# Optimization experiments

Measured on AMD Instinct MI355X. Metric: run time of the kernel, lower is better.

Reference implementation:

```python
import jax, jax.numpy as jnp
import numpy as np

B, S, D, H = 4, 2048, 1024, 16
DH = D // H


def setup_inputs() -> dict:
    key = jax.random.key(0)
    ks = jax.random.split(key, 10)
    init = lambda k, shape: jax.random.normal(k, shape, dtype=jnp.float32) * 0.02
    return {
        "x": jax.random.normal(ks[0], (B, S, D), dtype=jnp.float32),
        "attention_mask": jnp.ones((B, S), dtype=bool),
        "use_causal_mask": 1,
        "Wq": init(ks[1], (D, D)), "bq": jnp.zeros((D,), jnp.float32),
        "Wk": init(ks[2], (D, D)), "bk": jnp.zeros((D,), jnp.float32),
        "Wv": init(ks[3], (D, D)), "bv": jnp.zeros((D,), jnp.float32),
        "Wo": init(ks[4], (D, D)), "bo": jnp.zeros((D,), jnp.float32),
    }


def _split_heads(t):
    # (B, S, D) -> (B, H, S, DH)
    b, s, d = t.shape
    return t.reshape(b, s, H, DH).transpose(0, 2, 1, 3)


def reference(x, attention_mask, use_causal_mask, Wq, bq, Wk, bk, Wv, bv, Wo, bo):
    q = _split_heads(x @ Wq + bq)  # (B, H, S, DH)
    k = _split_heads(x @ Wk + bk)
    v = _split_heads(x @ Wv + bv)

    scale = 1.0 / jnp.sqrt(jnp.asarray(DH, dtype=x.dtype))
    scores = jnp.einsum("bhqd,bhkd->bhqk", q, k) * scale  # (B, H, S, S)

    blocked = jnp.finfo(scores.dtype).min
    if use_causal_mask:
        causal = jnp.tril(jnp.ones((S, S), dtype=bool))[None, None]
        scores = jnp.where(causal, scores, blocked)
    # attention_mask: (B, S) over keys
    scores = jnp.where(attention_mask[:, None, None, :], scores, blocked)

    weights = jax.nn.softmax(scores, axis=-1)
    attn = jnp.einsum("bhqk,bhkd->bhqd", weights, v)  # (B, H, S, DH)
    attn = attn.transpose(0, 2, 1, 3).reshape(B, S, D)  # combine heads
    return attn @ Wo + bo
```

## Files before the change

kernel.cpp:

```cpp
#include <hip/hip_runtime.h>
#include <hip/hip_bf16.h>
#include <cstdint>
#include <cstddef>


#define BB 4
#define SS 2048
#define DD 1024
#define HH 16
#define DHH 64

typedef float f32x4 __attribute__((ext_vector_type(4)));
typedef __bf16 bf16x8 __attribute__((ext_vector_type(8)));

#define QSCALE 0.1803368801111204f

__device__ __forceinline__ unsigned short f2bf(float f) {
  union { __hip_bfloat16 h; unsigned short u; } cv;
  cv.h = __float2bfloat16(f);
  return cv.u;
}

__device__ __forceinline__ float fexp2(float x) { return __builtin_amdgcn_exp2f(x); }

__device__ __forceinline__ void gload_lds16(const void* g, void* l) {
  __builtin_amdgcn_global_load_lds((const __attribute__((address_space(1))) void*)g,
                                   (__attribute__((address_space(3))) void*)l,
                                   16, 0, 0);
}

__global__ void k_f32_to_bf16(const float* __restrict__ in,
                              unsigned short* __restrict__ out, int n8) {
  int i = blockIdx.x * blockDim.x + threadIdx.x;
  if (i >= n8) return;
  const float4* p = (const float4*)in + (size_t)i * 2;
  float4 a = p[0], b = p[1];
  union { unsigned short u[8]; uint4 v; } r;
  r.u[0] = f2bf(a.x); r.u[1] = f2bf(a.y); r.u[2] = f2bf(a.z); r.u[3] = f2bf(a.w);
  r.u[4] = f2bf(b.x); r.u[5] = f2bf(b.y); r.u[6] = f2bf(b.z); r.u[7] = f2bf(b.w);
  ((uint4*)out)[i] = r.v;
}

__global__ void k_transpose_w4(const float* __restrict__ Wq, const float* __restrict__ Wk,
                               const float* __restrict__ Wv, const float* __restrict__ Wo,
                               unsigned short* __restrict__ Wqkvt,
                               unsigned short* __restrict__ Wot) {
  __shared__ float t[64][65];
  const int z = blockIdx.z;
  const float* W = (z == 0) ? Wq : (z == 1) ? Wk : (z == 2) ? Wv : Wo;
  unsigned short* dst = (z < 3) ? (Wqkvt + (size_t)z * DD * DD) : Wot;
  int bx = blockIdx.x * 64;
  int by = blockIdx.y * 64;
  int c  = threadIdx.x & 63;
  int r0 = threadIdx.x >> 6;
#pragma unroll
  for (int r = r0; r < 64; r += 4)
    t[r][c] = W[(size_t)(by + r) * DD + bx + c];
  __syncthreads();
#pragma unroll
  for (int r = r0; r < 64; r += 4)
    dst[(size_t)(bx + r) * DD + by + c] = f2bf(t[c][r]);
}

template <int MODE, int GN>
__global__ __launch_bounds__(256) void k_gemm(const unsigned short* __restrict__ A,
                                              const unsigned short* __restrict__ Bt,
                                              const float* __restrict__ b0,
                                              const float* __restrict__ b1,
                                              const float* __restrict__ b2,
                                              void* __restrict__ out0,
                                              void* __restrict__ out1,
                                              void* __restrict__ out2) {
  constexpr int Kd = 1024;
  __shared__ unsigned short As[128 * 64];
  __shared__ unsigned short Bs[128 * 64];
  const int tid = threadIdx.x;
  const int wave = tid >> 6, lane = tid & 63;
  const int hw = blockIdx.x;
  const int xcd = hw & 7;
  const int j = hw >> 3;
  const int super = j >> 6;
  const int rem = j & 63;
  const int bm = (xcd * 8 + (rem >> 3)) * 128;
  const int bn = (super * 8 + (rem & 7)) * 128;
  const int wm = (wave >> 1) * 64, wn = (wave & 1) * 64;

  f32x4 acc[4][4] = {};

  const int srow = wave * 8 + (lane >> 3);
  const int csw = lane & 7;

  for (int k0 = 0; k0 < Kd; k0 += 64) {
#pragma unroll
    for (int q = 0; q < 4; q++) {
      int r = q * 32 + srow;
      int clog = csw ^ (r & 7);
      gload_lds16(A + (size_t)(bm + r) * Kd + k0 + clog * 8, &As[q * 2048 + wave * 512]);
      gload_lds16(Bt + (size_t)(bn + r) * Kd + k0 + clog * 8, &Bs[q * 2048 + wave * 512]);
    }
    __syncthreads();
#pragma unroll
    for (int kk = 0; kk < 2; kk++) {
      bf16x8 af[4], bfr[4];
      int ch = (kk << 2) | (lane >> 4);
#pragma unroll
      for (int i = 0; i < 4; i++) {
        int row = wm + i * 16 + (lane & 15);
        af[i] = *(const bf16x8*)&As[row * 64 + ((ch ^ (row & 7)) << 3)];
      }
#pragma unroll
      for (int j2 = 0; j2 < 4; j2++) {
        int col = wn + j2 * 16 + (lane & 15);
        bfr[j2] = *(const bf16x8*)&Bs[col * 64 + ((ch ^ (col & 7)) << 3)];
      }
#pragma unroll
      for (int i = 0; i < 4; i++)
#pragma unroll
        for (int j2 = 0; j2 < 4; j2++)
          acc[i][j2] = __builtin_amdgcn_mfma_f32_16x16x32_bf16(af[i], bfr[j2], acc[i][j2], 0, 0, 0);
    }
    __syncthreads();
  }

  const int mat = bn >> 10;
  const float* bias = (MODE == 2) ? b0 : (mat == 0 ? b0 : (mat == 1 ? b1 : b2));
  const float scale = (MODE == 0 && mat == 0) ? QSCALE : 1.0f;
#pragma unroll
  for (int i = 0; i < 4; i++) {
#pragma unroll
    for (int j2 = 0; j2 < 4; j2++) {
      int col = bn + wn + j2 * 16 + (lane & 15);
      int c2 = col & 1023;
      float bv = bias[MODE == 2 ? col : c2];
      int row0 = bm + wm + i * 16 + ((lane >> 4) << 2);
      if (MODE == 0 && mat == 2) {
        int b = row0 >> 11, s0 = row0 & 2047, h = c2 >> 6, dh = c2 & 63;
        ushort4 pk;
        pk.x = f2bf(acc[i][j2][0] + bv);
        pk.y = f2bf(acc[i][j2][1] + bv);
        pk.z = f2bf(acc[i][j2][2] + bv);
        pk.w = f2bf(acc[i][j2][3] + bv);
        *(ushort4*)((unsigned short*)out2 + (((size_t)(b * HH + h) * DHH + dh) << 11) + s0) = pk;
      } else {
#pragma unroll
        for (int reg = 0; reg < 4; reg++) {
          int row = row0 + reg;
          float v = (acc[i][j2][reg] + bv) * scale;
          if (MODE == 0) {
            int b = row >> 11, s = row & 2047, h = c2 >> 6, dh = c2 & 63;
            unsigned short* dst = (unsigned short*)(mat == 0 ? out0 : out1);
            dst[(((size_t)(b * HH + h) * SS + s) << 6) + dh] = f2bf(v);
          } else {
            ((float*)out0)[(size_t)row * DD + col] = v;
          }
        }
      }
    }
  }
}

__global__ __launch_bounds__(256) void k_attn(const unsigned short* __restrict__ Q,
                                              const unsigned short* __restrict__ Kb,
                                              const unsigned short* __restrict__ Vt,
                                              unsigned short* __restrict__ O,
                                              const int* __restrict__ use_causal) {
  __shared__ unsigned short Ks[64 * 64];
  __shared__ unsigned short Vs[64 * 64];
  __shared__ unsigned short Ps[4 * 16 * 64];
  const int hw = blockIdx.x;
  const int bh = (hw & 7) | ((hw >> 7) << 3);
  const int pr = (hw >> 3) & 15;
  const int b = bh >> 4, h = bh & 15;
  const int tid = threadIdx.x, wave = tid >> 6, lane = tid & 63;
  const int lanelo = lane & 15, lanehi = lane >> 4;
  const bool causal = (use_causal[0] != 0);

  const unsigned short* Kg = Kb + (size_t)bh * SS * DHH;
  const unsigned short* Vg = Vt + (size_t)bh * DHH * SS;
  const int srow = wave * 8 + (lane >> 3);
  const int csw = lane & 7;
  const int qlocal = wave * 16 + lanelo;

  for (int pass = 0; pass < 2; pass++) {
    const int qt = pass ? (SS / 64 - 1 - pr) : pr;
    const unsigned short* Qg = Q + ((size_t)bh * SS + qt * 64) * DHH;

    bf16x8 qf0, qf1;
    {
      const unsigned short* qrow = Qg + (wave * 16 + lanelo) * DHH + (lanehi << 3);
      qf0 = *(const bf16x8*)qrow;
      qf1 = *(const bf16x8*)(qrow + 32);
    }

    float m = -1e30f, ls = 0.f;
    f32x4 o[4] = {};
    const int ntile = causal ? (qt + 1) : (SS / 64);

    for (int kt = 0; kt < ntile; kt++) {
#pragma unroll
      for (int q = 0; q < 2; q++) {
        int r = q * 32 + srow;
        int clog = csw ^ (r & 7);
        gload_lds16(Kg + (size_t)(kt * 64 + r) * DHH + clog * 8, &Ks[q * 2048 + wave * 512]);
        gload_lds16(Vg + (size_t)r * SS + kt * 64 + clog * 8, &Vs[q * 2048 + wave * 512]);
      }
      __syncthreads();

      f32x4 scT[4];
#pragma unroll
      for (int kb = 0; kb < 4; kb++) {
        int key = kb * 16 + lanelo;
        bf16x8 a0 = *(const bf16x8*)&Ks[key * 64 + ((lanehi ^ (key & 7)) << 3)];
        bf16x8 a1 = *(const bf16x8*)&Ks[key * 64 + (((lanehi + 4) ^ (key & 7)) << 3)];
        f32x4 t = {};
        t = __builtin_amdgcn_mfma_f32_16x16x32_bf16(a0, qf0, t, 0, 0, 0);
        t = __builtin_amdgcn_mfma_f32_16x16x32_bf16(a1, qf1, t, 0, 0, 0);
        scT[kb] = t;
      }

      const bool needmask = causal && (kt == qt);
      float mx = -3.0e38f;
#pragma unroll
      for (int kb = 0; kb < 4; kb++)
#pragma unroll
        for (int reg = 0; reg < 4; reg++) {
          float v = scT[kb][reg];
          if (needmask && (kb * 16 + 4 * lanehi + reg) > qlocal) v = -3.0e38f;
          scT[kb][reg] = v;
          mx = fmaxf(mx, v);
        }

      if (__any((int)(mx > m + 8.0f))) {
        float rmx = fmaxf(mx, __shfl_xor(mx, 16, 64));
        rmx = fmaxf(rmx, __shfl_xor(rmx, 32, 64));
        float mnew = fmaxf(m, rmx);
        float al = fexp2(m - mnew);
        m = mnew;
        ls *= al;
        float alr[4];
#pragma unroll
        for (int reg = 0; reg < 4; reg++)
          alr[reg] = __shfl(al, (lanehi << 2) + reg, 64);
#pragma unroll
        for (int dhb = 0; dhb < 4; dhb++) {
          f32x4 t = o[dhb];
          t[0] *= alr[0]; t[1] *= alr[1]; t[2] *= alr[2]; t[3] *= alr[3];
          o[dhb] = t;
        }
      }

      unsigned short* Pw = &Ps[wave * 1024];
#pragma unroll
      for (int kb = 0; kb < 4; kb++) {
        ushort4 pk;
        float p0 = fexp2(scT[kb][0] - m);
        float p1 = fexp2(scT[kb][1] - m);
        float p2 = fexp2(scT[kb][2] - m);
        float p3 = fexp2(scT[kb][3] - m);
        ls += (p0 + p1) + (p2 + p3);
        pk.x = f2bf(p0); pk.y = f2bf(p1); pk.z = f2bf(p2); pk.w = f2bf(p3);
        int chunk = (kb * 2 + (lanehi >> 1)) ^ (lanelo & 7);
        *(ushort4*)&Pw[lanelo * 64 + (chunk << 3) + ((lanehi & 1) << 2)] = pk;
      }

      int ar = lanelo;
      bf16x8 pa0 = *(const bf16x8*)&Pw[ar * 64 + ((lanehi ^ (ar & 7)) << 3)];
      bf16x8 pa1 = *(const bf16x8*)&Pw[ar * 64 + (((lanehi + 4) ^ (ar & 7)) << 3)];
#pragma unroll
      for (int dhb = 0; dhb < 4; dhb++) {
        int dh = dhb * 16 + lanelo;
        bf16x8 v0 = *(const bf16x8*)&Vs[dh * 64 + ((lanehi ^ (dh & 7)) << 3)];
        bf16x8 v1 = *(const bf16x8*)&Vs[dh * 64 + (((lanehi + 4) ^ (dh & 7)) << 3)];
        o[dhb] = __builtin_amdgcn_mfma_f32_16x16x32_bf16(pa0, v0, o[dhb], 0, 0, 0);
        o[dhb] = __builtin_amdgcn_mfma_f32_16x16x32_bf16(pa1, v1, o[dhb], 0, 0, 0);
      }
      __syncthreads();
    }

    float t = ls + __shfl_xor(ls, 16, 64);
    t += __shfl_xor(t, 32, 64);
    float inv = 1.0f / t;
    float invr[4];
#pragma unroll
    for (int reg = 0; reg < 4; reg++)
      invr[reg] = __shfl(inv, (lanehi << 2) + reg, 64);
#pragma unroll
    for (int dhb = 0; dhb < 4; dhb++)
#pragma unroll
      for (int reg = 0; reg < 4; reg++) {
        int s = qt * 64 + wave * 16 + (lanehi << 2) + reg;
        int dh = dhb * 16 + lanelo;
        O[((size_t)(b * SS + s)) * DD + h * DHH + dh] = f2bf(o[dhb][reg] * invr[reg]);
      }
  }
}

extern "C" void kernel_launch(void* const* d_in, const int* in_sizes, int n_in,
                              void* d_out, int out_size, void* d_ws, size_t ws_size,
                              hipStream_t stream) {
  const float* x = (const float*)d_in[0];
  const int* use_causal = (const int*)d_in[2];
  const float* Wq = (const float*)d_in[3];
  const float* bq = (const float*)d_in[4];
  const float* Wk = (const float*)d_in[5];
  const float* bk = (const float*)d_in[6];
  const float* Wv = (const float*)d_in[7];
  const float* bv = (const float*)d_in[8];
  const float* Wo = (const float*)d_in[9];
  const float* bo = (const float*)d_in[10];

  char* ws = (char*)d_ws;
  unsigned short* xb    = (unsigned short*)(ws);
  unsigned short* Wqkvt = (unsigned short*)(ws + (16ull << 20));
  unsigned short* Wot   = (unsigned short*)(ws + (22ull << 20));
  unsigned short* Qb    = (unsigned short*)(ws + (24ull << 20));
  unsigned short* Kbuf  = (unsigned short*)(ws + (40ull << 20));
  unsigned short* Vtb   = (unsigned short*)(ws + (56ull << 20));
  unsigned short* Attn  = (unsigned short*)(ws + (72ull << 20));

  int n8 = BB * SS * DD / 8;
  k_f32_to_bf16<<<(n8 + 255) / 256, 256, 0, stream>>>(x, xb, n8);

  k_transpose_w4<<<dim3(16, 16, 4), 256, 0, stream>>>(Wq, Wk, Wv, Wo, Wqkvt, Wot);

  k_gemm<0, 24><<<dim3(64 * 24), 256, 0, stream>>>(xb, Wqkvt, bq, bk, bv, Qb, Kbuf, Vtb);

  k_attn<<<dim3(1024), 256, 0, stream>>>(Qb, Kbuf, Vtb, Attn, use_causal);

  k_gemm<2, 8><<<dim3(64 * 8), 256, 0, stream>>>(Attn, Wot, bo, nullptr, nullptr, d_out, nullptr, nullptr);
}
```

Before: 177.4 us.

## Double-buffer LDS tiles in GEMM and attention with async prefetch

Both the projection GEMM and the attention kernel now keep two LDS buffers and issue the global-to-LDS loads for the next K tile before computing on the current one. Explicit vmcnt waits and raw s_barrier calls replace __syncthreads, so each wave waits only for the older loads. This is meant to hide global memory latency behind MFMA work. In exchange it doubles LDS use (GEMM goes to 64KB), which may lower occupancy, and correctness depends on the hand-counted vmcnt values and on LDS-DMA completion being ordered by vmcnt.

```diff
diff --git a/kernel.cpp b/kernel.cpp
--- a/kernel.cpp
+++ b/kernel.cpp
@@ -27,6 +27,15 @@
   __builtin_amdgcn_global_load_lds((const __attribute__((address_space(1))) void*)g,
                                    (__attribute__((address_space(3))) void*)l,
                                    16, 0, 0);
+}
+
+__device__ __forceinline__ void wait_vm4() { asm volatile("s_waitcnt vmcnt(4)" ::: "memory"); }
+__device__ __forceinline__ void wait_vm8() { asm volatile("s_waitcnt vmcnt(8)" ::: "memory"); }
+__device__ __forceinline__ void wait_vm0() { asm volatile("s_waitcnt vmcnt(0)" ::: "memory"); }
+__device__ __forceinline__ void block_barrier() {
+  asm volatile("" ::: "memory");
+  __builtin_amdgcn_s_barrier();
+  asm volatile("" ::: "memory");
 }
 
 __global__ void k_f32_to_bf16(const float* __restrict__ in,
@@ -72,8 +81,9 @@
                                               void* __restrict__ out1,
                                               void* __restrict__ out2) {
   constexpr int Kd = 1024;
-  __shared__ unsigned short As[128 * 64];
-  __shared__ unsigned short Bs[128 * 64];
+  constexpr int NSTEP = Kd / 64;
+  __shared__ unsigned short As[2][128 * 64];
+  __shared__ unsigned short Bs[2][128 * 64];
   const int tid = threadIdx.x;
   const int wave = tid >> 6, lane = tid & 63;
   const int hw = blockIdx.x;
@@ -90,15 +100,27 @@
   const int srow = wave * 8 + (lane >> 3);
   const int csw = lane & 7;
 
-  for (int k0 = 0; k0 < Kd; k0 += 64) {
+  auto stage = [&](int buf, int k0) {
 #pragma unroll
     for (int q = 0; q < 4; q++) {
       int r = q * 32 + srow;
       int clog = csw ^ (r & 7);
-      gload_lds16(A + (size_t)(bm + r) * Kd + k0 + clog * 8, &As[q * 2048 + wave * 512]);
-      gload_lds16(Bt + (size_t)(bn + r) * Kd + k0 + clog * 8, &Bs[q * 2048 + wave * 512]);
-    }
-    __syncthreads();
+      gload_lds16(A + (size_t)(bm + r) * Kd + k0 + clog * 8, &As[buf][q * 2048 + wave * 512]);
+      gload_lds16(Bt + (size_t)(bn + r) * Kd + k0 + clog * 8, &Bs[buf][q * 2048 + wave * 512]);
+    }
+  };
+
+  stage(0, 0);
+  for (int ks = 0; ks < NSTEP; ks++) {
+    if (ks + 1 < NSTEP) {
+      stage((ks + 1) & 1, (ks + 1) * 64);
+      wait_vm8();
+    } else {
+      wait_vm0();
+    }
+    block_barrier();
+    const unsigned short* Asb = As[ks & 1];
+    const unsigned short* Bsb = Bs[ks & 1];
 #pragma unroll
     for (int kk = 0; kk < 2; kk++) {
       bf16x8 af[4], bfr[4];
@@ -106,12 +128,12 @@
 #pragma unroll
       for (int i = 0; i < 4; i++) {
         int row = wm + i * 16 + (lane & 15);
-        af[i] = *(const bf16x8*)&As[row * 64 + ((ch ^ (row & 7)) << 3)];
+        af[i] = *(const bf16x8*)&Asb[row * 64 + ((ch ^ (row & 7)) << 3)];
       }
 #pragma unroll
       for (int j2 = 0; j2 < 4; j2++) {
         int col = wn + j2 * 16 + (lane & 15);
-        bfr[j2] = *(const bf16x8*)&Bs[col * 64 + ((ch ^ (col & 7)) << 3)];
+        bfr[j2] = *(const bf16x8*)&Bsb[col * 64 + ((ch ^ (col & 7)) << 3)];
       }
 #pragma unroll
       for (int i = 0; i < 4; i++)
@@ -119,7 +141,7 @@
         for (int j2 = 0; j2 < 4; j2++)
           acc[i][j2] = __builtin_amdgcn_mfma_f32_16x16x32_bf16(af[i], bfr[j2], acc[i][j2], 0, 0, 0);
     }
-    __syncthreads();
+    block_barrier();
   }
 
   const int mat = bn >> 10;
@@ -164,8 +186,8 @@
                                               const unsigned short* __restrict__ Vt,
                                               unsigned short* __restrict__ O,
                                               const int* __restrict__ use_causal) {
-  __shared__ unsigned short Ks[64 * 64];
-  __shared__ unsigned short Vs[64 * 64];
+  __shared__ unsigned short Ks[2][64 * 64];
+  __shared__ unsigned short Vs[2][64 * 64];
   __shared__ unsigned short Ps[4 * 16 * 64];
   const int hw = blockIdx.x;
   const int bh = (hw & 7) | ((hw >> 7) << 3);
@@ -181,6 +203,16 @@
   const int csw = lane & 7;
   const int qlocal = wave * 16 + lanelo;
 
+  auto stage = [&](int buf, int kt) {
+#pragma unroll
+    for (int q = 0; q < 2; q++) {
+      int r = q * 32 + srow;
+      int clog = csw ^ (r & 7);
+      gload_lds16(Kg + (size_t)(kt * 64 + r) * DHH + clog * 8, &Ks[buf][q * 2048 + wave * 512]);
+      gload_lds16(Vg + (size_t)r * SS + kt * 64 + clog * 8, &Vs[buf][q * 2048 + wave * 512]);
+    }
+  };
+
   for (int pass = 0; pass < 2; pass++) {
     const int qt = pass ? (SS / 64 - 1 - pr) : pr;
     const unsigned short* Qg = Q + ((size_t)bh * SS + qt * 64) * DHH;
@@ -196,22 +228,24 @@
     f32x4 o[4] = {};
     const int ntile = causal ? (qt + 1) : (SS / 64);
 
+    stage(0, 0);
     for (int kt = 0; kt < ntile; kt++) {
-#pragma unroll
-      for (int q = 0; q < 2; q++) {
-        int r = q * 32 + srow;
-        int clog = csw ^ (r & 7);
-        gload_lds16(Kg + (size_t)(kt * 64 + r) * DHH + clog * 8, &Ks[q * 2048 + wave * 512]);
-        gload_lds16(Vg + (size_t)r * SS + kt * 64 + clog * 8, &Vs[q * 2048 + wave * 512]);
-      }
-      __syncthreads();
+      if (kt + 1 < ntile) {
+        stage((kt + 1) & 1, kt + 1);
+        wait_vm4();
+      } else {
+        wait_vm0();
+      }
+      block_barrier();
+      const unsigned short* Ksb = Ks[kt & 1];
+      const unsigned short* Vsb = Vs[kt & 1];
 
       f32x4 scT[4];
 #pragma unroll
       for (int kb = 0; kb < 4; kb++) {
         int key = kb * 16 + lanelo;
-        bf16x8 a0 = *(const bf16x8*)&Ks[key * 64 + ((lanehi ^ (key & 7)) << 3)];
-        bf16x8 a1 = *(const bf16x8*)&Ks[key * 64 + (((lanehi + 4) ^ (key & 7)) << 3)];
+        bf16x8 a0 = *(const bf16x8*)&Ksb[key * 64 + ((lanehi ^ (key & 7)) << 3)];
+        bf16x8 a1 = *(const bf16x8*)&Ksb[key * 64 + (((lanehi + 4) ^ (key & 7)) << 3)];
         f32x4 t = {};
         t = __builtin_amdgcn_mfma_f32_16x16x32_bf16(a0, qf0, t, 0, 0, 0);
         t = __builtin_amdgcn_mfma_f32_16x16x32_bf16(a1, qf1, t, 0, 0, 0);
@@ -269,12 +303,12 @@
 #pragma unroll
       for (int dhb = 0; dhb < 4; dhb++) {
         int dh = dhb * 16 + lanelo;
-        bf16x8 v0 = *(const bf16x8*)&Vs[dh * 64 + ((lanehi ^ (dh & 7)) << 3)];
-        bf16x8 v1 = *(const bf16x8*)&Vs[dh * 64 + (((lanehi + 4) ^ (dh & 7)) << 3)];
+        bf16x8 v0 = *(const bf16x8*)&Vsb[dh * 64 + ((lanehi ^ (dh & 7)) << 3)];
+        bf16x8 v1 = *(const bf16x8*)&Vsb[dh * 64 + (((lanehi + 4) ^ (dh & 7)) << 3)];
         o[dhb] = __builtin_amdgcn_mfma_f32_16x16x32_bf16(pa0, v0, o[dhb], 0, 0, 0);
         o[dhb] = __builtin_amdgcn_mfma_f32_16x16x32_bf16(pa1, v1, o[dhb], 0, 0, 0);
       }
-      __syncthreads();
+      block_barrier();
     }
 
     float t = ls + __shfl_xor(ls, 16, 64);
```

New measurement: 173.6 us. -2.1%, faster.
